# Optimization experiments

Hardware: AMD Instinct MI355X
Metric: run time of the kernel (lower is better)

The kernel has to match this reference:

```python
import jax, jax.numpy as jnp
import numpy as np

B, N, D, M, C = 4, 256, 128, 128, 128


def _lin_init(key, din, dout):
    # torch nn.Linear default: U(-1/sqrt(din), 1/sqrt(din)) for weight and bias
    bound = 1.0 / np.sqrt(din)
    kw, kb = jax.random.split(key)
    W = jax.random.uniform(kw, (din, dout), jnp.float32, -bound, bound)
    b = jax.random.uniform(kb, (dout,), jnp.float32, -bound, bound)
    return W, b


def setup_inputs() -> dict:
    key = jax.random.key(0)
    k_h, k_adj, k1, k2, k3, k4 = jax.random.split(key, 6)
    h = jax.random.normal(k_h, (B, N, D), jnp.float32)
    adj = jax.random.uniform(k_adj, (B, N, N), jnp.float32)
    # msg MLP: Linear(2D -> M), SiLU, Linear(M -> M). Split first weight into
    # the h_i block (W1a) and h_j block (W1b) of the concatenated input.
    W1, b1 = _lin_init(k1, 2 * D, M)
    W1a, W1b = W1[:D], W1[D:]
    W2, b2 = _lin_init(k2, M, M)
    # to_c MLP: Linear(M -> M), SiLU, Linear(M -> C)
    Wc1, bc1 = _lin_init(k3, M, M)
    Wc2, bc2 = _lin_init(k4, M, C)
    return {"h": h, "adj": adj, "W1a": W1a, "W1b": W1b, "b1": b1,
            "W2": W2, "b2": b2, "Wc1": Wc1, "bc1": bc1, "Wc2": Wc2, "bc2": bc2}


def reference(h, adj, W1a, W1b, b1, W2, b2, Wc1, bc1, Wc2, bc2):
    n = h.shape[1]
    # First msg Linear on cat([h_i, h_j]) == h_i @ W1a + h_j @ W1b + b1.
    # Precompute per-node projections once instead of the (B,N,N,2D) pair tensor.
    pi = jnp.einsum('bnd,dm->bnm', h, W1a)           # (B,N,M) for destination i
    pj = jnp.einsum('bnd,dm->bnm', h, W1b)           # (B,N,M) for source j
    pre = pi[:, :, None, :] + pj[:, None, :, :] + b1  # (B,N,N,M)
    m = jnp.einsum('bijm,mk->bijk', jax.nn.silu(pre), W2) + b2  # (B,N,N,M)
    # zero self-messages (diagonal ignored), then weight by adjacency
    mask = (1.0 - jnp.eye(n, dtype=h.dtype))[None, :, :, None]
    m = m * mask * adj[..., None]
    # mean aggregation over source nodes j with clamped degree
    denom = jnp.clip(jnp.sum(adj, axis=-1, keepdims=True), 1.0)  # (B,N,1)
    m_agg = jnp.sum(m, axis=2) / denom                           # (B,N,M)
    c = jnp.einsum('bnm,mc->bnc', jax.nn.silu(jnp.einsum('bnm,mk->bnk', m_agg, Wc1) + bc1), Wc2) + bc2
    return c
```

## Files before the change

### kernel.cpp

```cpp
#include <hip/hip_runtime.h>
#include <math.h>

#define BB 4
#define NN 256
#define DD 128
#define MM 128
#define CC 128
#define ROWS (BB * NN)

static __device__ __forceinline__ float fast_exp2(float x) {
#if __has_builtin(__builtin_amdgcn_exp2f)
    return __builtin_amdgcn_exp2f(x);
#else
    return __exp2f(x);
#endif
}

static __device__ __forceinline__ float fast_rcp(float x) {
#if __has_builtin(__builtin_amdgcn_rcpf)
    return __builtin_amdgcn_rcpf(x);
#else
    return 1.0f / x;
#endif
}

static __device__ __forceinline__ float silu_f(float x) {
    float e = fast_exp2(-1.44269504088896340736f * x);
    return x * fast_rcp(1.0f + e);
}

__global__ __launch_bounds__(256) void k_proj(const float* __restrict__ h,
                                              const float* __restrict__ W1a,
                                              const float* __restrict__ W1b,
                                              const float* __restrict__ b1,
                                              float* __restrict__ pibias,
                                              float* __restrict__ pj) {
    __shared__ float sWa[32 * MM];
    __shared__ float sWb[32 * MM];
    __shared__ float sH[2 * DD];

    const int t = threadIdx.x;
    const int m = t & 127;
    const int r = t >> 7;
    const int row0 = blockIdx.x * 2;

    const float bias = b1[m];

    sH[t] = h[(size_t)row0 * DD + t];

    float accA = 0.0f, accB = 0.0f;
    for (int c = 0; c < 4; ++c) {
        __syncthreads();
        const float4* ga = (const float4*)(W1a + (size_t)c * 32 * MM);
        const float4* gb = (const float4*)(W1b + (size_t)c * 32 * MM);
        float4* la = (float4*)sWa;
        float4* lb = (float4*)sWb;
        #pragma unroll
        for (int i = 0; i < 4; ++i) {
            la[t + 256 * i] = ga[t + 256 * i];
            lb[t + 256 * i] = gb[t + 256 * i];
        }
        __syncthreads();

        #pragma unroll 8
        for (int dd = 0; dd < 32; ++dd) {
            const int d = c * 32 + dd;
            const float hv = sH[r * DD + d];
            accA = fmaf(hv, sWa[dd * MM + m], accA);
            accB = fmaf(hv, sWb[dd * MM + m], accB);
        }
    }

    const int row = row0 + r;
    pibias[(size_t)row * MM + m] = accA + bias;
    pj[(size_t)row * MM + m]     = accB;
}

__global__ __launch_bounds__(256) void k_msgout(const float* __restrict__ adj,
                                                const float* __restrict__ pibias,
                                                const float* __restrict__ pj,
                                                const float* __restrict__ W2,
                                                const float* __restrict__ b2,
                                                const float* __restrict__ Wc1,
                                                const float* __restrict__ bc1,
                                                const float* __restrict__ Wc2,
                                                const float* __restrict__ bc2,
                                                float* __restrict__ out) {
    __shared__ float sStage[64 * MM];
    __shared__ float sAdj[2][NN];
    __shared__ float sRed[2][256];
    __shared__ float sS[2 * MM];
    __shared__ float sB[2 * MM];
    __shared__ float sWred[2][4];

    const int t = threadIdx.x;
    const int blk = blockIdx.x;
    const int b = blk >> 7;
    const int i0 = (blk & 127) * 2;
    const int row0 = b * NN + i0;

    const int m = t & 127;
    const int half = t >> 7;

    const float b2k  = b2[m];
    const float bc1k = bc1[m];
    const float bc2k = bc2[m];
    const float pim0 = pibias[(size_t)row0 * MM + m];
    const float pim1 = pibias[(size_t)(row0 + 1) * MM + m];

    const float* arow = adj + (size_t)row0 * NN;
    const float a0v = arow[t];
    const float a1v = arow[t + 256];
    sAdj[0][t] = a0v;
    sAdj[1][t] = a1v;
    __syncthreads();

    float v0 = a0v, v1 = a1v;
    #pragma unroll
    for (int off = 32; off > 0; off >>= 1) {
        v0 += __shfl_xor(v0, off, 64);
        v1 += __shfl_xor(v1, off, 64);
    }
    if ((t & 63) == 0) { sWred[0][t >> 6] = v0; sWred[1][t >> 6] = v1; }
    __syncthreads();
    const float A0 = sWred[0][0] + sWred[0][1] + sWred[0][2] + sWred[0][3];
    const float A1 = sWred[1][0] + sWred[1][1] + sWred[1][2] + sWred[1][3];
    const float aii0 = sAdj[0][i0];
    const float aii1 = sAdj[1][i0 + 1];
    __syncthreads();
    if (t == 0) { sAdj[0][i0] = 0.0f; sAdj[1][i0 + 1] = 0.0f; }

    const float inv0 = 1.0f / fmaxf(A0, 1.0f);
    const float inv1 = 1.0f / fmaxf(A1, 1.0f);
    const float bet0 = (A0 - aii0) * inv0;
    const float bet1 = (A1 - aii1) * inv1;

    const float* __restrict__ pjB = pj + (size_t)b * NN * MM;
    float acc0 = 0.0f, acc1 = 0.0f;
    for (int c = 0; c < 4; ++c) {
        __syncthreads();
        const float4* g = (const float4*)(pjB + (size_t)c * 64 * MM);
        float4* l = (float4*)sStage;
        #pragma unroll
        for (int i = 0; i < 8; ++i) l[t + 256 * i] = g[t + 256 * i];
        __syncthreads();

        #pragma unroll 8
        for (int jj = half; jj < 64; jj += 2) {
            const int j = c * 64 + jj;
            const float pjv = sStage[jj * MM + m];
            const float w0 = sAdj[0][j];
            const float w1 = sAdj[1][j];
            acc0 = fmaf(w0, silu_f(pim0 + pjv), acc0);
            acc1 = fmaf(w1, silu_f(pim1 + pjv), acc1);
        }
    }

    sRed[0][t] = acc0;
    sRed[1][t] = acc1;
    __syncthreads();
    if (t < 128) {
        sS[t] = (sRed[0][t] + sRed[0][t + 128]) * inv0;
    } else {
        const int k = t - 128;
        sS[MM + k] = (sRed[1][k] + sRed[1][k + 128]) * inv1;
    }

    const float betr = (half == 0) ? bet0 : bet1;

    float acc = betr * b2k;
    for (int c = 0; c < 2; ++c) {
        __syncthreads();
        const float4* g = (const float4*)(W2 + (size_t)c * 64 * MM);
        float4* l = (float4*)sStage;
        #pragma unroll
        for (int i = 0; i < 8; ++i) l[t + 256 * i] = g[t + 256 * i];
        __syncthreads();
        #pragma unroll 8
        for (int dd = 0; dd < 64; ++dd) {
            const int d = c * 64 + dd;
            acc = fmaf(sS[half * MM + d], sStage[dd * MM + m], acc);
        }
    }
    sB[half * MM + m] = acc;

    acc = bc1k;
    for (int c = 0; c < 2; ++c) {
        __syncthreads();
        const float4* g = (const float4*)(Wc1 + (size_t)c * 64 * MM);
        float4* l = (float4*)sStage;
        #pragma unroll
        for (int i = 0; i < 8; ++i) l[t + 256 * i] = g[t + 256 * i];
        __syncthreads();
        #pragma unroll 8
        for (int dd = 0; dd < 64; ++dd) {
            const int d = c * 64 + dd;
            acc = fmaf(sB[half * MM + d], sStage[dd * MM + m], acc);
        }
    }
    __syncthreads();
    sS[half * MM + m] = silu_f(acc);

    acc = bc2k;
    for (int c = 0; c < 2; ++c) {
        __syncthreads();
        const float4* g = (const float4*)(Wc2 + (size_t)c * 64 * MM);
        float4* l = (float4*)sStage;
        #pragma unroll
        for (int i = 0; i < 8; ++i) l[t + 256 * i] = g[t + 256 * i];
        __syncthreads();
        #pragma unroll 8
        for (int dd = 0; dd < 64; ++dd) {
            const int d = c * 64 + dd;
            acc = fmaf(sS[half * MM + d], sStage[dd * MM + m], acc);
        }
    }
    out[(size_t)(row0 + half) * CC + m] = acc;
}

extern "C" void kernel_launch(void* const* d_in, const int* in_sizes, int n_in,
                              void* d_out, int out_size, void* d_ws, size_t ws_size,
                              hipStream_t stream) {
    const float* h   = (const float*)d_in[0];
    const float* adj = (const float*)d_in[1];
    const float* W1a = (const float*)d_in[2];
    const float* W1b = (const float*)d_in[3];
    const float* b1  = (const float*)d_in[4];
    const float* W2  = (const float*)d_in[5];
    const float* b2  = (const float*)d_in[6];
    const float* Wc1 = (const float*)d_in[7];
    const float* bc1 = (const float*)d_in[8];
    const float* Wc2 = (const float*)d_in[9];
    const float* bc2 = (const float*)d_in[10];
    float* out = (float*)d_out;

    float* ws = (float*)d_ws;
    float* pibias = ws;
    float* pj     = ws + (size_t)ROWS * MM;

    k_proj<<<ROWS / 2, 256, 0, stream>>>(h, W1a, W1b, b1, pibias, pj);
    k_msgout<<<ROWS / 2, 256, 0, stream>>>(adj, pibias, pj, W2, b2, Wc1, bc1,
                                           Wc2, bc2, out);
}
```

Baseline: 102.8 us.

## Fuse projection and message kernels into one cooperative kernel with grid syncs

Merges the node-projection kernel and the message/output kernel into a single cooperative launch. pi is kept in shared memory and pj is written into the output buffer as scratch, with grid-wide syncs separating the phases. This removes one kernel launch and the pi round trip through global memory. In exchange it needs all 512 blocks co-resident and adds two grid barriers, the second of which looks unnecessary. It falls back to the two-kernel path if the cooperative launch fails.

New measurement: 198.7 us. 93.2% more time.

```diff
diff --git a/kernel.cpp b/kernel.cpp
--- a/kernel.cpp
+++ b/kernel.cpp
@@ -1,5 +1,8 @@
 #include <hip/hip_runtime.h>
+#include <hip/hip_cooperative_groups.h>
 #include <math.h>
+
+namespace cg = cooperative_groups;
 
 #define BB 4
 #define NN 256
@@ -27,6 +30,182 @@
 static __device__ __forceinline__ float silu_f(float x) {
     float e = fast_exp2(-1.44269504088896340736f * x);
     return x * fast_rcp(1.0f + e);
+}
+
+__global__ __launch_bounds__(256) void k_fused(const float* __restrict__ h,
+                                               const float* __restrict__ adj,
+                                               const float* __restrict__ W1a,
+                                               const float* __restrict__ W1b,
+                                               const float* __restrict__ b1,
+                                               const float* __restrict__ W2,
+                                               const float* __restrict__ b2,
+                                               const float* __restrict__ Wc1,
+                                               const float* __restrict__ bc1,
+                                               const float* __restrict__ Wc2,
+                                               const float* __restrict__ bc2,
+                                               float* __restrict__ out) {
+    __shared__ float sStage[64 * MM];
+    __shared__ float sAdj[2][NN];
+    __shared__ float sRed[2][256];
+    __shared__ float sS[2 * MM];
+    __shared__ float sB[2 * MM];
+    __shared__ float sPi[2 * MM];
+    __shared__ float sH[2 * DD];
+    __shared__ float sWred[2][4];
+
+    const int t = threadIdx.x;
+    const int blk = blockIdx.x;
+    const int b = blk >> 7;
+    const int i0 = (blk & 127) * 2;
+    const int row0 = b * NN + i0;
+
+    const int m = t & 127;
+    const int half = t >> 7;
+
+    sH[t] = h[(size_t)row0 * DD + t];
+    const float bias = b1[m];
+
+    float accA = 0.0f, accB = 0.0f;
+    for (int c = 0; c < 4; ++c) {
+        __syncthreads();
+        const float4* ga = (const float4*)(W1a + (size_t)c * 32 * MM);
+        const float4* gb = (const float4*)(W1b + (size_t)c * 32 * MM);
+        float4* la = (float4*)sStage;
+        float4* lb = (float4*)(sStage + 32 * MM);
+        #pragma unroll
+        for (int i = 0; i < 4; ++i) {
+            la[t + 256 * i] = ga[t + 256 * i];
+            lb[t + 256 * i] = gb[t + 256 * i];
+        }
+        __syncthreads();
+
+        #pragma unroll 8
+        for (int dd = 0; dd < 32; ++dd) {
+            const int d = c * 32 + dd;
+            const float hv = sH[half * DD + d];
+            accA = fmaf(hv, sStage[dd * MM + m], accA);
+            accB = fmaf(hv, sStage[32 * MM + dd * MM + m], accB);
+        }
+    }
+    sPi[half * MM + m] = accA + bias;
+    out[(size_t)(row0 + half) * MM + m] = accB;
+
+    const float* arow = adj + (size_t)row0 * NN;
+    const float a0v = arow[t];
+    const float a1v = arow[t + 256];
+    sAdj[0][t] = a0v;
+    sAdj[1][t] = a1v;
+
+    float v0 = a0v, v1 = a1v;
+    #pragma unroll
+    for (int off = 32; off > 0; off >>= 1) {
+        v0 += __shfl_xor(v0, off, 64);
+        v1 += __shfl_xor(v1, off, 64);
+    }
+    if ((t & 63) == 0) { sWred[0][t >> 6] = v0; sWred[1][t >> 6] = v1; }
+    __syncthreads();
+    const float A0 = sWred[0][0] + sWred[0][1] + sWred[0][2] + sWred[0][3];
+    const float A1 = sWred[1][0] + sWred[1][1] + sWred[1][2] + sWred[1][3];
+    const float aii0 = sAdj[0][i0];
+    const float aii1 = sAdj[1][i0 + 1];
+    const float pim0 = sPi[m];
+    const float pim1 = sPi[MM + m];
+    __syncthreads();
+    if (t == 0) { sAdj[0][i0] = 0.0f; sAdj[1][i0 + 1] = 0.0f; }
+
+    const float inv0 = 1.0f / fmaxf(A0, 1.0f);
+    const float inv1 = 1.0f / fmaxf(A1, 1.0f);
+    const float bet0 = (A0 - aii0) * inv0;
+    const float bet1 = (A1 - aii1) * inv1;
+
+    cg::this_grid().sync();
+
+    const float* __restrict__ pjB = out + (size_t)b * NN * MM;
+    float acc0 = 0.0f, acc1 = 0.0f;
+    for (int c = 0; c < 4; ++c) {
+        __syncthreads();
+        const float4* g = (const float4*)(pjB + (size_t)c * 64 * MM);
+        float4* l = (float4*)sStage;
+        #pragma unroll
+        for (int i = 0; i < 8; ++i) l[t + 256 * i] = g[t + 256 * i];
+        __syncthreads();
+
+        #pragma unroll 8
+        for (int jj = half; jj < 64; jj += 2) {
+            const int j = c * 64 + jj;
+            const float pjv = sStage[jj * MM + m];
+            const float w0 = sAdj[0][j];
+            const float w1 = sAdj[1][j];
+            acc0 = fmaf(w0, silu_f(pim0 + pjv), acc0);
+            acc1 = fmaf(w1, silu_f(pim1 + pjv), acc1);
+        }
+    }
+
+    sRed[0][t] = acc0;
+    sRed[1][t] = acc1;
+    __syncthreads();
+    if (t < 128) {
+        sS[t] = (sRed[0][t] + sRed[0][t + 128]) * inv0;
+    } else {
+        const int k = t - 128;
+        sS[MM + k] = (sRed[1][k] + sRed[1][k + 128]) * inv1;
+    }
+
+    cg::this_grid().sync();
+
+    const float b2k  = b2[m];
+    const float bc1k = bc1[m];
+    const float bc2k = bc2[m];
+    const float betr = (half == 0) ? bet0 : bet1;
+
+    float acc = betr * b2k;
+    for (int c = 0; c < 2; ++c) {
+        __syncthreads();
+        const float4* g = (const float4*)(W2 + (size_t)c * 64 * MM);
+        float4* l = (float4*)sStage;
+        #pragma unroll
+        for (int i = 0; i < 8; ++i) l[t + 256 * i] = g[t + 256 * i];
+        __syncthreads();
+        #pragma unroll 8
+        for (int dd = 0; dd < 64; ++dd) {
+            const int d = c * 64 + dd;
+            acc = fmaf(sS[half * MM + d], sStage[dd * MM + m], acc);
+        }
+    }
+    sB[half * MM + m] = acc;
+
+    acc = bc1k;
+    for (int c = 0; c < 2; ++c) {
+        __syncthreads();
+        const float4* g = (const float4*)(Wc1 + (size_t)c * 64 * MM);
+        float4* l = (float4*)sStage;
+        #pragma unroll
+        for (int i = 0; i < 8; ++i) l[t + 256 * i] = g[t + 256 * i];
+        __syncthreads();
+        #pragma unroll 8
+        for (int dd = 0; dd < 64; ++dd) {
+            const int d = c * 64 + dd;
+            acc = fmaf(sB[half * MM + d], sStage[dd * MM + m], acc);
+        }
+    }
+    __syncthreads();
+    sS[half * MM + m] = silu_f(acc);
+
+    acc = bc2k;
+    for (int c = 0; c < 2; ++c) {
+        __syncthreads();
+        const float4* g = (const float4*)(Wc2 + (size_t)c * 64 * MM);
+        float4* l = (float4*)sStage;
+        #pragma unroll
+        for (int i = 0; i < 8; ++i) l[t + 256 * i] = g[t + 256 * i];
+        __syncthreads();
+        #pragma unroll 8
+        for (int dd = 0; dd < 64; ++dd) {
+            const int d = c * 64 + dd;
+            acc = fmaf(sS[half * MM + d], sStage[dd * MM + m], acc);
+        }
+    }
+    out[(size_t)(row0 + half) * CC + m] = acc;
 }
 
 __global__ __launch_bounds__(256) void k_proj(const float* __restrict__ h,
@@ -45,7 +224,6 @@
     const int row0 = blockIdx.x * 2;
 
     const float bias = b1[m];
-
     sH[t] = h[(size_t)row0 * DD + t];
 
     float accA = 0.0f, accB = 0.0f;
@@ -234,11 +412,19 @@
     const float* bc2 = (const float*)d_in[10];
     float* out = (float*)d_out;
 
-    float* ws = (float*)d_ws;
-    float* pibias = ws;
-    float* pj     = ws + (size_t)ROWS * MM;
-
-    k_proj<<<ROWS / 2, 256, 0, stream>>>(h, W1a, W1b, b1, pibias, pj);
-    k_msgout<<<ROWS / 2, 256, 0, stream>>>(adj, pibias, pj, W2, b2, Wc1, bc1,
-                                           Wc2, bc2, out);
-}
+    void* args[] = {(void*)&h,   (void*)&adj, (void*)&W1a, (void*)&W1b,
+                    (void*)&b1,  (void*)&W2,  (void*)&b2,  (void*)&Wc1,
+                    (void*)&bc1, (void*)&Wc2, (void*)&bc2, (void*)&out};
+    hipError_t err = hipLaunchCooperativeKernel((const void*)k_fused,
+                                                dim3(ROWS / 2), dim3(256),
+                                                args, 0, stream);
+
+    if (err != hipSuccess) {
+        float* ws = (float*)d_ws;
+        float* pibias = ws;
+        float* pj     = ws + (size_t)ROWS * MM;
+        k_proj<<<ROWS / 2, 256, 0, stream>>>(h, W1a, W1b, b1, pibias, pj);
+        k_msgout<<<ROWS / 2, 256, 0, stream>>>(adj, pibias, pj, W2, b2, Wc1,
+                                               bc1, Wc2, bc2, out);
+    }
+}
```

## Process four rows per block with 512 threads and fold the SiLU exponent

Applied to the files above, without the earlier changes.

Both kernels now use 512-thread blocks covering four destination rows instead of two. Each staged tile of pj and of the weights in shared memory is therefore reused across twice as many rows, halving the global-to-LDS traffic per row. In the message loop every thread now walks all 64 sources for a single row, which removes the two-way j split and the cross-half reduction through shared memory. The -log2(e)*pi term is also hoisted so the exponent is one FMA. The cost is half as many blocks (256), which may leave many compute units idle, plus larger per-block LDS use in k_proj.

Measured after the change: 99.29 us. 1.04x faster.

```diff
diff --git a/kernel.cpp b/kernel.cpp
--- a/kernel.cpp
+++ b/kernel.cpp
@@ -7,6 +7,9 @@
 #define MM 128
 #define CC 128
 #define ROWS (BB * NN)
+#define RPB 4
+#define NBLK (ROWS / RPB)
+#define TPB 512
 
 static __device__ __forceinline__ float fast_exp2(float x) {
 #if __has_builtin(__builtin_amdgcn_exp2f)
@@ -29,54 +32,52 @@
     return x * fast_rcp(1.0f + e);
 }
 
-__global__ __launch_bounds__(256) void k_proj(const float* __restrict__ h,
+__global__ __launch_bounds__(TPB) void k_proj(const float* __restrict__ h,
                                               const float* __restrict__ W1a,
                                               const float* __restrict__ W1b,
                                               const float* __restrict__ b1,
                                               float* __restrict__ pibias,
                                               float* __restrict__ pj) {
-    __shared__ float sWa[32 * MM];
-    __shared__ float sWb[32 * MM];
-    __shared__ float sH[2 * DD];
+    __shared__ float sWa[64 * MM];
+    __shared__ float sWb[64 * MM];
+    __shared__ float sH[RPB * DD];
 
     const int t = threadIdx.x;
     const int m = t & 127;
-    const int r = t >> 7;
-    const int row0 = blockIdx.x * 2;
+    const int q = t >> 7;
+    const int row0 = blockIdx.x * RPB;
 
     const float bias = b1[m];
 
     sH[t] = h[(size_t)row0 * DD + t];
 
     float accA = 0.0f, accB = 0.0f;
-    for (int c = 0; c < 4; ++c) {
-        __syncthreads();
-        const float4* ga = (const float4*)(W1a + (size_t)c * 32 * MM);
-        const float4* gb = (const float4*)(W1b + (size_t)c * 32 * MM);
+    for (int c = 0; c < 2; ++c) {
+        __syncthreads();
+        const float4* ga = (const float4*)(W1a + (size_t)c * 64 * MM);
+        const float4* gb = (const float4*)(W1b + (size_t)c * 64 * MM);
         float4* la = (float4*)sWa;
         float4* lb = (float4*)sWb;
         #pragma unroll
         for (int i = 0; i < 4; ++i) {
-            la[t + 256 * i] = ga[t + 256 * i];
-            lb[t + 256 * i] = gb[t + 256 * i];
-        }
-        __syncthreads();
-
-        #pragma unroll 8
-        for (int dd = 0; dd < 32; ++dd) {
-            const int d = c * 32 + dd;
-            const float hv = sH[r * DD + d];
+            la[t + TPB * i] = ga[t + TPB * i];
+            lb[t + TPB * i] = gb[t + TPB * i];
+        }
+        __syncthreads();
+
+        #pragma unroll 8
+        for (int dd = 0; dd < 64; ++dd) {
+            const float hv = sH[q * DD + c * 64 + dd];
             accA = fmaf(hv, sWa[dd * MM + m], accA);
             accB = fmaf(hv, sWb[dd * MM + m], accB);
         }
     }
 
-    const int row = row0 + r;
-    pibias[(size_t)row * MM + m] = accA + bias;
-    pj[(size_t)row * MM + m]     = accB;
-}
-
-__global__ __launch_bounds__(256) void k_msgout(const float* __restrict__ adj,
+    pibias[(size_t)row0 * MM + t] = accA + bias;
+    pj[(size_t)row0 * MM + t]     = accB;
+}
+
+__global__ __launch_bounds__(TPB) void k_msgout(const float* __restrict__ adj,
                                                 const float* __restrict__ pibias,
                                                 const float* __restrict__ pj,
                                                 const float* __restrict__ W2,
@@ -87,33 +88,33 @@
                                                 const float* __restrict__ bc2,
                                                 float* __restrict__ out) {
     __shared__ float sStage[64 * MM];
-    __shared__ float sAdj[2][NN];
-    __shared__ float sRed[2][256];
-    __shared__ float sS[2 * MM];
-    __shared__ float sB[2 * MM];
-    __shared__ float sWred[2][4];
+    __shared__ float sAdj[RPB][NN];
+    __shared__ float sS[RPB * MM];
+    __shared__ float sB[RPB * MM];
+    __shared__ float sWred0[8];
+    __shared__ float sWred1[8];
 
     const int t = threadIdx.x;
     const int blk = blockIdx.x;
-    const int b = blk >> 7;
-    const int i0 = (blk & 127) * 2;
+    const int b = blk >> 6;
+    const int i0 = (blk & 63) * RPB;
     const int row0 = b * NN + i0;
 
     const int m = t & 127;
-    const int half = t >> 7;
+    const int q = t >> 7;
+    const int w = t >> 6;
 
     const float b2k  = b2[m];
     const float bc1k = bc1[m];
     const float bc2k = bc2[m];
-    const float pim0 = pibias[(size_t)row0 * MM + m];
-    const float pim1 = pibias[(size_t)(row0 + 1) * MM + m];
+    const float pim  = pibias[(size_t)(row0 + q) * MM + m];
 
     const float* arow = adj + (size_t)row0 * NN;
     const float a0v = arow[t];
-    const float a1v = arow[t + 256];
-    sAdj[0][t] = a0v;
-    sAdj[1][t] = a1v;
-    __syncthreads();
+    const float a1v = arow[t + TPB];
+    float* sA = &sAdj[0][0];
+    sA[t] = a0v;
+    sA[t + TPB] = a1v;
 
     float v0 = a0v, v1 = a1v;
     #pragma unroll
@@ -121,101 +122,91 @@
         v0 += __shfl_xor(v0, off, 64);
         v1 += __shfl_xor(v1, off, 64);
     }
-    if ((t & 63) == 0) { sWred[0][t >> 6] = v0; sWred[1][t >> 6] = v1; }
+    if ((t & 63) == 0) { sWred0[w] = v0; sWred1[w] = v1; }
     __syncthreads();
-    const float A0 = sWred[0][0] + sWred[0][1] + sWred[0][2] + sWred[0][3];
-    const float A1 = sWred[1][0] + sWred[1][1] + sWred[1][2] + sWred[1][3];
-    const float aii0 = sAdj[0][i0];
-    const float aii1 = sAdj[1][i0 + 1];
+
+    float A;
+    if (q < 2) {
+        const int base = (q & 1) * 4;
+        A = sWred0[base] + sWred0[base + 1] + sWred0[base + 2] + sWred0[base + 3];
+    } else {
+        const int base = (q & 1) * 4;
+        A = sWred1[base] + sWred1[base + 1] + sWred1[base + 2] + sWred1[base + 3];
+    }
+    const float aii = sAdj[q][i0 + q];
     __syncthreads();
-    if (t == 0) { sAdj[0][i0] = 0.0f; sAdj[1][i0 + 1] = 0.0f; }
-
-    const float inv0 = 1.0f / fmaxf(A0, 1.0f);
-    const float inv1 = 1.0f / fmaxf(A1, 1.0f);
-    const float bet0 = (A0 - aii0) * inv0;
-    const float bet1 = (A1 - aii1) * inv1;
+    if (t < RPB) sAdj[t][i0 + t] = 0.0f;
+
+    const float inv  = 1.0f / fmaxf(A, 1.0f);
+    const float bet  = (A - aii) * inv;
+    const float npim = -1.44269504088896340736f * pim;
 
     const float* __restrict__ pjB = pj + (size_t)b * NN * MM;
-    float acc0 = 0.0f, acc1 = 0.0f;
+    float acc = 0.0f;
     for (int c = 0; c < 4; ++c) {
         __syncthreads();
         const float4* g = (const float4*)(pjB + (size_t)c * 64 * MM);
         float4* l = (float4*)sStage;
         #pragma unroll
-        for (int i = 0; i < 8; ++i) l[t + 256 * i] = g[t + 256 * i];
-        __syncthreads();
-
-        #pragma unroll 8
-        for (int jj = half; jj < 64; jj += 2) {
-            const int j = c * 64 + jj;
+        for (int i = 0; i < 4; ++i) l[t + TPB * i] = g[t + TPB * i];
+        __syncthreads();
+
+        #pragma unroll 8
+        for (int jj = 0; jj < 64; ++jj) {
             const float pjv = sStage[jj * MM + m];
-            const float w0 = sAdj[0][j];
-            const float w1 = sAdj[1][j];
-            acc0 = fmaf(w0, silu_f(pim0 + pjv), acc0);
-            acc1 = fmaf(w1, silu_f(pim1 + pjv), acc1);
-        }
-    }
-
-    sRed[0][t] = acc0;
-    sRed[1][t] = acc1;
-    __syncthreads();
-    if (t < 128) {
-        sS[t] = (sRed[0][t] + sRed[0][t + 128]) * inv0;
-    } else {
-        const int k = t - 128;
-        sS[MM + k] = (sRed[1][k] + sRed[1][k + 128]) * inv1;
-    }
-
-    const float betr = (half == 0) ? bet0 : bet1;
-
-    float acc = betr * b2k;
+            const float wgt = sAdj[q][c * 64 + jj];
+            const float x   = pim + pjv;
+            const float e   = fast_exp2(fmaf(-1.44269504088896340736f, pjv, npim));
+            acc = fmaf(wgt, x * fast_rcp(1.0f + e), acc);
+        }
+    }
+    sS[q * MM + m] = acc * inv;
+
+
+    float acc2 = bet * b2k;
     for (int c = 0; c < 2; ++c) {
         __syncthreads();
         const float4* g = (const float4*)(W2 + (size_t)c * 64 * MM);
         float4* l = (float4*)sStage;
         #pragma unroll
-        for (int i = 0; i < 8; ++i) l[t + 256 * i] = g[t + 256 * i];
-        __syncthreads();
-        #pragma unroll 8
-        for (int dd = 0; dd < 64; ++dd) {
-            const int d = c * 64 + dd;
-            acc = fmaf(sS[half * MM + d], sStage[dd * MM + m], acc);
-        }
-    }
-    sB[half * MM + m] = acc;
-
-    acc = bc1k;
+        for (int i = 0; i < 4; ++i) l[t + TPB * i] = g[t + TPB * i];
+        __syncthreads();
+        #pragma unroll 8
+        for (int dd = 0; dd < 64; ++dd) {
+            acc2 = fmaf(sS[q * MM + c * 64 + dd], sStage[dd * MM + m], acc2);
+        }
+    }
+    sB[q * MM + m] = acc2;
+
+    acc2 = bc1k;
     for (int c = 0; c < 2; ++c) {
         __syncthreads();
         const float4* g = (const float4*)(Wc1 + (size_t)c * 64 * MM);
         float4* l = (float4*)sStage;
         #pragma unroll
-        for (int i = 0; i < 8; ++i) l[t + 256 * i] = g[t + 256 * i];
-        __syncthreads();
-        #pragma unroll 8
-        for (int dd = 0; dd < 64; ++dd) {
-            const int d = c * 64 + dd;
-            acc = fmaf(sB[half * MM + d], sStage[dd * MM + m], acc);
-        }
-    }
-    __syncthreads();
-    sS[half * MM + m] = silu_f(acc);
-
-    acc = bc2k;
+        for (int i = 0; i < 4; ++i) l[t + TPB * i] = g[t + TPB * i];
+        __syncthreads();
+        #pragma unroll 8
+        for (int dd = 0; dd < 64; ++dd) {
+            acc2 = fmaf(sB[q * MM + c * 64 + dd], sStage[dd * MM + m], acc2);
+        }
+    }
+    sS[q * MM + m] = silu_f(acc2);
+
+    acc2 = bc2k;
     for (int c = 0; c < 2; ++c) {
         __syncthreads();
         const float4* g = (const float4*)(Wc2 + (size_t)c * 64 * MM);
         float4* l = (float4*)sStage;
         #pragma unroll
-        for (int i = 0; i < 8; ++i) l[t + 256 * i] = g[t + 256 * i];
-        __syncthreads();
-        #pragma unroll 8
-        for (int dd = 0; dd < 64; ++dd) {
-            const int d = c * 64 + dd;
-            acc = fmaf(sS[half * MM + d], sStage[dd * MM + m], acc);
-        }
-    }
-    out[(size_t)(row0 + half) * CC + m] = acc;
+        for (int i = 0; i < 4; ++i) l[t + TPB * i] = g[t + TPB * i];
+        __syncthreads();
+        #pragma unroll 8
+        for (int dd = 0; dd < 64; ++dd) {
+            acc2 = fmaf(sS[q * MM + c * 64 + dd], sStage[dd * MM + m], acc2);
+        }
+    }
+    out[(size_t)row0 * CC + t] = acc2;
 }
 
 extern "C" void kernel_launch(void* const* d_in, const int* in_sizes, int n_in,
@@ -238,7 +229,7 @@
     float* pibias = ws;
     float* pj     = ws + (size_t)ROWS * MM;
 
-    k_proj<<<ROWS / 2, 256, 0, stream>>>(h, W1a, W1b, b1, pibias, pj);
-    k_msgout<<<ROWS / 2, 256, 0, stream>>>(adj, pibias, pj, W2, b2, Wc1, bc1,
-                                           Wc2, bc2, out);
-}
+    k_proj<<<NBLK, TPB, 0, stream>>>(h, W1a, W1b, b1, pibias, pj);
+    k_msgout<<<NBLK, TPB, 0, stream>>>(adj, pibias, pj, W2, b2, Wc1, bc1,
+                                       Wc2, bc2, out);
+}
```
